# Performance work log

Hardware: AMD Instinct MI355X
Metric: run time of the kernel (lower is better)

The kernel has to match this reference:

```python
import jax, jax.numpy as jnp
import numpy as np

HID = 32

def setup_inputs() -> dict:
    key = jax.random.key(0)
    ks = jax.random.split(key, 20)
    N, F, C, E = 100000, 128, 10, 3200000
    x = jax.random.normal(ks[0], (N, F), dtype=jnp.float32)
    edge_index = jax.random.randint(ks[1], (2, E), 0, N, dtype=jnp.int64)
    edge_weight = jax.random.uniform(ks[2], (E,), dtype=jnp.float32)
    H = jnp.zeros((N, HID), dtype=jnp.float32)
    s = 1.0 / np.sqrt(F)
    t = 1.0 / np.sqrt(2 * HID)
    u = 1.0 / np.sqrt(HID)
    p = {
        'Wz': jax.random.normal(ks[3], (F, HID)) * s,  'bz': jnp.zeros((HID,)),
        'Wr': jax.random.normal(ks[4], (F, HID)) * s,  'br': jnp.zeros((HID,)),
        'Wh': jax.random.normal(ks[5], (F, HID)) * s,  'bh': jnp.zeros((HID,)),
        'Lz_w': jax.random.normal(ks[6], (2 * HID, HID)) * t, 'Lz_b': jnp.zeros((HID,)),
        'Lr_w': jax.random.normal(ks[7], (2 * HID, HID)) * t, 'Lr_b': jnp.zeros((HID,)),
        'Lh_w': jax.random.normal(ks[8], (2 * HID, HID)) * t, 'Lh_b': jnp.zeros((HID,)),
        'lin_w': jax.random.normal(ks[9], (HID, C)) * u,      'lin_b': jnp.zeros((C,)),
    }
    return {'x': x, 'edge_index': edge_index, 'edge_weight': edge_weight, 'H': H, **p}


def reference(x, edge_index, edge_weight, H,
              Wz, bz, Wr, br, Wh, bh,
              Lz_w, Lz_b, Lr_w, Lr_b, Lh_w, Lh_b,
              lin_w, lin_b):
    N = x.shape[0]
    # gcn_norm with self-loops (fill value 1), symmetric normalization
    loop = jnp.arange(N, dtype=edge_index.dtype)
    src = jnp.concatenate([edge_index[0], loop])
    dst = jnp.concatenate([edge_index[1], loop])
    w = jnp.concatenate([edge_weight, jnp.ones((N,), edge_weight.dtype)])
    deg = jax.ops.segment_sum(w, dst, num_segments=N)
    dinv = jnp.where(deg > 0, jax.lax.rsqrt(deg), 0.0)
    norm = dinv[src] * w * dinv[dst]  # [E+N]

    def gcn(W, b):
        xw = x @ W  # [N, HID]
        msg = xw[src] * norm[:, None]  # gather + scale
        return jax.ops.segment_sum(msg, dst, num_segments=N) + b

    Z = jax.nn.sigmoid(jnp.concatenate([gcn(Wz, bz), H], axis=1) @ Lz_w + Lz_b)
    R = jax.nn.sigmoid(jnp.concatenate([gcn(Wr, br), H], axis=1) @ Lr_w + Lr_b)
    H_tilde = jnp.tanh(jnp.concatenate([gcn(Wh, bh), H * R], axis=1) @ Lh_w + Lh_b)
    H_new = Z * H + (1.0 - Z) * H_tilde

    h = jax.nn.relu(H_new)
    logits = h @ lin_w + lin_b
    return (jax.nn.softmax(logits, axis=1), H)
```

## Files before the change

### kernel.cpp

```cpp
#include <hip/hip_runtime.h>
#include <cstdint>
#include <cmath>

#define HID 32
#define GATES 96
#define F 128
#define NB_MAX 512
#define CH 4096
#define STAGE_CAP 9000

typedef float nfloat2 __attribute__((ext_vector_type(2)));

__device__ inline unsigned f2b(float x) {
    unsigned u = __float_as_uint(x);
    return (u + 0x7FFFu + ((u >> 16) & 1u)) >> 16;
}


__global__ __launch_bounds__(256) void k_bcount(const int* __restrict__ ei_dst,
        unsigned* __restrict__ bCnt, int E, int nb) {
    __shared__ unsigned h[NB_MAX];
    for (int i = threadIdx.x; i < NB_MAX; i += 256) h[i] = 0;
    __syncthreads();
    for (int e = blockIdx.x * 256 + threadIdx.x; e < E; e += gridDim.x * 256)
        atomicAdd(&h[((const unsigned*)ei_dst)[e] >> 8], 1u);
    __syncthreads();
    for (int b = threadIdx.x; b < nb; b += 256)
        if (h[b]) atomicAdd(&bCnt[b], h[b]);
}

__global__ __launch_bounds__(512) void k_bscan(const unsigned* __restrict__ bCnt,
        unsigned* __restrict__ bOff, unsigned* __restrict__ bPos, int nb) {
    __shared__ unsigned s[512];
    int t = threadIdx.x;
    unsigned v = (t < nb) ? bCnt[t] : 0u;
    s[t] = v;
    __syncthreads();
    for (int o = 1; o < 512; o <<= 1) {
        unsigned x = s[t];
        if (t >= o) x += s[t - o];
        __syncthreads();
        s[t] = x;
        __syncthreads();
    }
    if (t < nb) { unsigned ex = s[t] - v; bOff[t] = ex; bPos[t] = ex; }
}

__global__ __launch_bounds__(256) void k_bscatter(const int* __restrict__ ei,
        const float* __restrict__ w, unsigned* __restrict__ bPos,
        float2* __restrict__ bsorted, int E) {
    __shared__ unsigned h[NB_MAX], base[NB_MAX];
    int c0 = blockIdx.x * CH;
    int c1 = c0 + CH; if (c1 > E) c1 = E;
    for (int i = threadIdx.x; i < NB_MAX; i += 256) h[i] = 0;
    __syncthreads();
    for (int e = c0 + threadIdx.x; e < c1; e += 256)
        atomicAdd(&h[((const unsigned*)ei)[(size_t)E + e] >> 8], 1u);
    __syncthreads();
    for (int b = threadIdx.x; b < NB_MAX; b += 256) {
        base[b] = h[b] ? atomicAdd(&bPos[b], h[b]) : 0u;
        h[b] = 0;
    }
    __syncthreads();
    for (int e = c0 + threadIdx.x; e < c1; e += 256) {
        unsigned d = ((const unsigned*)ei)[(size_t)E + e];
        unsigned b = d >> 8;
        unsigned r = atomicAdd(&h[b], 1u);
        unsigned pack = (unsigned)ei[e] | ((d & 255u) << 24);
        bsorted[base[b] + r] = make_float2(__int_as_float((int)pack), w[e]);
    }
}

__global__ __launch_bounds__(256) void k_bfine(const float2* __restrict__ bsorted,
        const unsigned* __restrict__ bOff,
        float2* __restrict__ sorted, unsigned* __restrict__ cnt, unsigned* __restrict__ off,
        float* __restrict__ dinv, int N, int E, int nb) {
    __shared__ float2 stage[STAGE_CAP];
    __shared__ unsigned h[256], h2[256], loc[256];
    __shared__ float wsum[256];
    int b = blockIdx.x, t = threadIdx.x;
    unsigned lo = bOff[b];
    unsigned hi = (b + 1 < nb) ? bOff[b + 1] : (unsigned)E;
    unsigned len = hi - lo;
    unsigned stlen = len < STAGE_CAP ? len : STAGE_CAP;
    h[t] = 0; h2[t] = 0; wsum[t] = 0.0f;
    __syncthreads();
    for (unsigned i = t; i < stlen; i += 256) {
        float2 e = bsorted[lo + i];
        stage[i] = e;
        unsigned ld = ((unsigned)__float_as_int(e.x)) >> 24;
        atomicAdd(&h[ld], 1u);
        atomicAdd(&wsum[ld], e.y);
    }
    for (unsigned i = stlen + t; i < len; i += 256) {
        float2 e = bsorted[lo + i];
        unsigned ld = ((unsigned)__float_as_int(e.x)) >> 24;
        atomicAdd(&h[ld], 1u);
        atomicAdd(&wsum[ld], e.y);
    }
    __syncthreads();
    unsigned v = h[t];
    loc[t] = v;
    __syncthreads();
    for (int o = 1; o < 256; o <<= 1) {
        unsigned x = loc[t];
        if (t >= o) x += loc[t - o];
        __syncthreads();
        loc[t] = x;
        __syncthreads();
    }
    unsigned ex = loc[t] - v;
    __syncthreads();
    loc[t] = ex;
    __syncthreads();
    int d = b * 256 + t;
    if (d < N) {
        cnt[d] = v;
        off[d] = lo + ex;
        dinv[d] = rsqrtf(1.0f + wsum[t]);
    }
    for (unsigned i = t; i < stlen; i += 256) {
        float2 e = stage[i];
        unsigned u = (unsigned)__float_as_int(e.x);
        unsigned ld = u >> 24;
        unsigned r = atomicAdd(&h2[ld], 1u);
        sorted[lo + loc[ld] + r] = make_float2(__int_as_float((int)(u & 0xFFFFFFu)), e.y);
    }
    for (unsigned i = stlen + t; i < len; i += 256) {
        float2 e = bsorted[lo + i];
        unsigned u = (unsigned)__float_as_int(e.x);
        unsigned ld = u >> 24;
        unsigned r = atomicAdd(&h2[ld], 1u);
        sorted[lo + loc[ld] + r] = make_float2(__int_as_float((int)(u & 0xFFFFFFu)), e.y);
    }
}

#define GR 16
__global__ __launch_bounds__(256) void k_gemm(const float* __restrict__ x,
        const float* __restrict__ Wz, const float* __restrict__ Wr, const float* __restrict__ Wh,
        const float* __restrict__ dinv, unsigned* __restrict__ xwh, int N) {
    __shared__ float Wl[F * GATES];
    __shared__ float xs[GR][F + 1];
    int tid = threadIdx.x;
    for (int i = tid; i < F * GATES; i += 256) {
        int k = i / GATES, c = i % GATES;
        float v;
        if (c < 32)      v = Wz[k * 32 + c];
        else if (c < 64) v = Wr[k * 32 + (c - 32)];
        else             v = Wh[k * 32 + (c - 64)];
        Wl[i] = v;
    }
    int r_local = tid / 16;
    int cb = tid % 16;
    int ntiles = (N + GR - 1) / GR;
    for (int t = blockIdx.x; t < ntiles; t += gridDim.x) {
        int row0 = t * GR;
        __syncthreads();
        for (int i = tid; i < GR * F; i += 256) {
            int r = i / F, k = i % F;
            int g = row0 + r;
            xs[r][k] = (g < N) ? x[(size_t)g * F + k] : 0.0f;
        }
        __syncthreads();
        int grow = row0 + r_local;
        if (grow < N) {
            float acc[6] = {0, 0, 0, 0, 0, 0};
            for (int k = 0; k < F; ++k) {
                float xv = xs[r_local][k];
                const float* wr = &Wl[k * GATES + cb * 6];
                #pragma unroll
                for (int j = 0; j < 6; ++j) acc[j] += xv * wr[j];
            }
            float dv = dinv[grow];
            unsigned* o = xwh + (size_t)grow * 48 + cb * 3;
            o[0] = f2b(dv * acc[0]) | (f2b(dv * acc[1]) << 16);
            o[1] = f2b(dv * acc[2]) | (f2b(dv * acc[3]) << 16);
            o[2] = f2b(dv * acc[4]) | (f2b(dv * acc[5]) << 16);
        }
    }
}

__global__ __launch_bounds__(256, 8) void k_fused(
        const unsigned* __restrict__ off, const unsigned* __restrict__ cnt,
        const float2* __restrict__ sorted,
        const unsigned* __restrict__ xwh, const float* __restrict__ dinv, const float* __restrict__ Hin,
        const float* __restrict__ bz, const float* __restrict__ br, const float* __restrict__ bh,
        const float* __restrict__ Lzw, const float* __restrict__ Lzb,
        const float* __restrict__ Lrw, const float* __restrict__ Lrb,
        const float* __restrict__ Lhw, const float* __restrict__ Lhb,
        const float* __restrict__ linw, const float* __restrict__ linb,
        float* __restrict__ out_probs, float* __restrict__ out_H, int N) {
    int tid = threadIdx.x;
    int l = tid & 31;
    int half = l >> 4;
    int q = l & 15;
    int n = blockIdx.x * 8 + (tid >> 5);
    if (n >= N) return;

    float di = dinv[n];
    float acc0 = 0, acc1 = 0, acc2 = 0, acc3 = 0, acc4 = 0, acc5 = 0;

    unsigned base = off[n], len = cnt[n];
    const nfloat2* mp = (const nfloat2*)sorted + base;
    unsigned j = half;
    #pragma unroll 2
    for (; j + 2 < len; j += 4) {
        nfloat2 ea = mp[j];
        nfloat2 eb = mp[j + 2];
        int   sa = __float_as_int(ea.x);
        int   sb = __float_as_int(eb.x);
        float ma = ea.y;
        float mb = eb.y;
        const unsigned* pa = xwh + (size_t)sa * 48 + q * 3;
        const unsigned* pb = xwh + (size_t)sb * 48 + q * 3;
        unsigned a0 = pa[0], a1 = pa[1], a2 = pa[2];
        unsigned b0 = pb[0], b1 = pb[1], b2 = pb[2];
        acc0 += ma * __uint_as_float(a0 << 16);
        acc1 += ma * __uint_as_float(a0 & 0xFFFF0000u);
        acc2 += ma * __uint_as_float(a1 << 16);
        acc3 += ma * __uint_as_float(a1 & 0xFFFF0000u);
        acc4 += ma * __uint_as_float(a2 << 16);
        acc5 += ma * __uint_as_float(a2 & 0xFFFF0000u);
        acc0 += mb * __uint_as_float(b0 << 16);
        acc1 += mb * __uint_as_float(b0 & 0xFFFF0000u);
        acc2 += mb * __uint_as_float(b1 << 16);
        acc3 += mb * __uint_as_float(b1 & 0xFFFF0000u);
        acc4 += mb * __uint_as_float(b2 << 16);
        acc5 += mb * __uint_as_float(b2 & 0xFFFF0000u);
    }
    for (; j < len; j += 2) {
        nfloat2 e = mp[j];
        int   s = __float_as_int(e.x);
        float m = e.y;
        const unsigned* p = xwh + (size_t)s * 48 + q * 3;
        unsigned u0 = p[0], u1 = p[1], u2 = p[2];
        acc0 += m * __uint_as_float(u0 << 16);
        acc1 += m * __uint_as_float(u0 & 0xFFFF0000u);
        acc2 += m * __uint_as_float(u1 << 16);
        acc3 += m * __uint_as_float(u1 & 0xFFFF0000u);
        acc4 += m * __uint_as_float(u2 << 16);
        acc5 += m * __uint_as_float(u2 & 0xFFFF0000u);
    }
    acc0 += __shfl_xor(acc0, 16, 32);
    acc1 += __shfl_xor(acc1, 16, 32);
    acc2 += __shfl_xor(acc2, 16, 32);
    acc3 += __shfl_xor(acc3, 16, 32);
    acc4 += __shfl_xor(acc4, 16, 32);
    acc5 += __shfl_xor(acc5, 16, 32);
    float g0, g1, g2, g3, g4, g5;
    {
        const unsigned* p = xwh + (size_t)n * 48 + q * 3;
        unsigned u0 = p[0], u1 = p[1], u2 = p[2];
        #define BIAS(f) ((f) < 32 ? bz[(f)] : ((f) < 64 ? br[(f) - 32] : bh[(f) - 64]))
        int f = q * 6;
        g0 = di * (acc0 + __uint_as_float(u0 << 16))         + BIAS(f);
        g1 = di * (acc1 + __uint_as_float(u0 & 0xFFFF0000u)) + BIAS(f + 1);
        g2 = di * (acc2 + __uint_as_float(u1 << 16))         + BIAS(f + 2);
        g3 = di * (acc3 + __uint_as_float(u1 & 0xFFFF0000u)) + BIAS(f + 3);
        g4 = di * (acc4 + __uint_as_float(u2 << 16))         + BIAS(f + 4);
        g5 = di * (acc5 + __uint_as_float(u2 & 0xFFFF0000u)) + BIAS(f + 5);
        #undef BIAS
    }
    #define GATHERF(out, fexp) { int ff = (fexp); int mm = ff / 6, ii = ff % 6;            \
        float t0 = __shfl(g0, mm, 32), t1 = __shfl(g1, mm, 32), t2 = __shfl(g2, mm, 32),   \
              t3 = __shfl(g3, mm, 32), t4 = __shfl(g4, mm, 32), t5 = __shfl(g5, mm, 32);   \
        out = ii == 0 ? t0 : ii == 1 ? t1 : ii == 2 ? t2 : ii == 3 ? t3 : ii == 4 ? t4 : t5; }
    float gz, gr, gh;
    GATHERF(gz, l);
    GATHERF(gr, 32 + l);
    GATHERF(gh, 64 + l);
    #undef GATHERF

    float Hd = Hin[(size_t)n * HID + l];

    float az = Lzb[l], ar = Lrb[l];
    #pragma unroll 4
    for (int k = 0; k < 32; ++k) {
        float gzk = __shfl(gz, k, 32);
        float grk = __shfl(gr, k, 32);
        float Hk  = __shfl(Hd, k, 32);
        az += gzk * Lzw[k * 32 + l] + Hk * Lzw[(32 + k) * 32 + l];
        ar += grk * Lrw[k * 32 + l] + Hk * Lrw[(32 + k) * 32 + l];
    }
    float Z  = 1.0f / (1.0f + __expf(-az));
    float Rg = 1.0f / (1.0f + __expf(-ar));
    float HR = Hd * Rg;
    float ah = Lhb[l];
    #pragma unroll 4
    for (int k = 0; k < 32; ++k) {
        float ghk = __shfl(gh, k, 32);
        float HRk = __shfl(HR, k, 32);
        ah += ghk * Lhw[k * 32 + l] + HRk * Lhw[(32 + k) * 32 + l];
    }
    float Ht = tanhf(ah);
    float Hn = Z * Hd + (1.0f - Z) * Ht;
    float h = fmaxf(Hn, 0.0f);

    float logit = (l < 10) ? linb[l] : -INFINITY;
    #pragma unroll 4
    for (int k = 0; k < 32; ++k) {
        float hk = __shfl(h, k, 32);
        if (l < 10) logit += hk * linw[k * 10 + l];
    }
    float mx = logit;
    #pragma unroll
    for (int o = 8; o >= 1; o >>= 1) mx = fmaxf(mx, __shfl_xor(mx, o, 16));
    float ex = (l < 10) ? __expf(logit - mx) : 0.0f;
    float sum = ex;
    #pragma unroll
    for (int o = 8; o >= 1; o >>= 1) sum += __shfl_xor(sum, o, 16);
    if (l < 10) out_probs[(size_t)n * 10 + l] = ex / sum;
    out_H[(size_t)n * HID + l] = Hd;
}

extern "C" void kernel_launch(void* const* d_in, const int* in_sizes, int n_in,
                              void* d_out, int out_size, void* d_ws, size_t ws_size,
                              hipStream_t stream) {
    const float* x    = (const float*)d_in[0];
    const int*   ei   = (const int*)d_in[1];
    const float* ew   = (const float*)d_in[2];
    const float* H    = (const float*)d_in[3];
    const float* Wz   = (const float*)d_in[4];
    const float* bz   = (const float*)d_in[5];
    const float* Wr   = (const float*)d_in[6];
    const float* br   = (const float*)d_in[7];
    const float* Wh   = (const float*)d_in[8];
    const float* bh   = (const float*)d_in[9];
    const float* Lzw  = (const float*)d_in[10];
    const float* Lzb  = (const float*)d_in[11];
    const float* Lrw  = (const float*)d_in[12];
    const float* Lrb  = (const float*)d_in[13];
    const float* Lhw  = (const float*)d_in[14];
    const float* Lhb  = (const float*)d_in[15];
    const float* linw = (const float*)d_in[16];
    const float* linb = (const float*)d_in[17];

    int N = in_sizes[0] / F;
    int E = in_sizes[2];
    int nb = (N + 255) / 256;

    float* ws = (float*)d_ws;
    unsigned* xwh     = (unsigned*)ws;
    float2*   sorted  = (float2*)(ws + (size_t)N * 48);
    float2*   bsorted = sorted + (size_t)E;
    float*    dinv    = (float*)(bsorted + (size_t)E);
    unsigned* cnt     = (unsigned*)(dinv + N);
    unsigned* off     = cnt + N;
    unsigned* bCnt    = off + N;
    unsigned* bOff    = bCnt + NB_MAX;
    unsigned* bPos    = bOff + NB_MAX;

    float* out_probs = (float*)d_out;
    float* out_H     = (float*)d_out + (size_t)N * 10;

    hipMemsetAsync(bCnt, 0, NB_MAX * sizeof(unsigned), stream);
    k_bcount<<<512, 256, 0, stream>>>(ei + (size_t)E, bCnt, E, nb);
    k_bscan<<<1, 512, 0, stream>>>(bCnt, bOff, bPos, nb);
    k_bscatter<<<(E + CH - 1) / CH, 256, 0, stream>>>(ei, ew, bPos, bsorted, E);
    k_bfine<<<nb, 256, 0, stream>>>(bsorted, bOff, sorted, cnt, off, dinv, N, E, nb);
    k_gemm<<<2048, 256, 0, stream>>>(x, Wz, Wr, Wh, dinv, xwh, N);
    k_fused<<<(N + 7) / 8, 256, 0, stream>>>(off, cnt, sorted, xwh, dinv, H,
                                             bz, br, bh, Lzw, Lzb, Lrw, Lrb, Lhw, Lhb,
                                             linw, linb, out_probs, out_H, N);
}
```

Before: 410.0 us.

## Fold bucket scan into scatter/fine kernels, cache dst in registers, widen aggregation to 64 lanes

```diff
diff --git a/kernel.cpp b/kernel.cpp
--- a/kernel.cpp
+++ b/kernel.cpp
@@ -7,6 +7,7 @@
 #define F 128
 #define NB_MAX 512
 #define CH 4096
+#define EPT 16
 #define STAGE_CAP 9000
 
 typedef float nfloat2 __attribute__((ext_vector_type(2)));
@@ -15,6 +16,8 @@
     unsigned u = __float_as_uint(x);
     return (u + 0x7FFFu + ((u >> 16) & 1u)) >> 16;
 }
+__device__ inline float blo(unsigned u) { return __uint_as_float(u << 16); }
+__device__ inline float bhi(unsigned u) { return __uint_as_float(u & 0xFFFF0000u); }
 
 
 __global__ __launch_bounds__(256) void k_bcount(const int* __restrict__ ei_dst,
@@ -29,59 +32,76 @@
         if (h[b]) atomicAdd(&bCnt[b], h[b]);
 }
 
-__global__ __launch_bounds__(512) void k_bscan(const unsigned* __restrict__ bCnt,
-        unsigned* __restrict__ bOff, unsigned* __restrict__ bPos, int nb) {
-    __shared__ unsigned s[512];
+__device__ inline void local_bscan(const unsigned* __restrict__ bCnt,
+        unsigned* __restrict__ boff, unsigned* __restrict__ ps) {
     int t = threadIdx.x;
-    unsigned v = (t < nb) ? bCnt[t] : 0u;
-    s[t] = v;
-    __syncthreads();
-    for (int o = 1; o < 512; o <<= 1) {
-        unsigned x = s[t];
-        if (t >= o) x += s[t - o];
-        __syncthreads();
-        s[t] = x;
-        __syncthreads();
-    }
-    if (t < nb) { unsigned ex = s[t] - v; bOff[t] = ex; bPos[t] = ex; }
+    unsigned c0 = bCnt[2 * t], c1 = bCnt[2 * t + 1];
+    unsigned pv = c0 + c1;
+    ps[t] = pv;
+    __syncthreads();
+    for (int o = 1; o < 256; o <<= 1) {
+        unsigned x = ps[t];
+        if (t >= o) x += ps[t - o];
+        __syncthreads();
+        ps[t] = x;
+        __syncthreads();
+    }
+    unsigned pex = ps[t] - pv;
+    boff[2 * t] = pex;
+    boff[2 * t + 1] = pex + c0;
+    __syncthreads();
 }
 
 __global__ __launch_bounds__(256) void k_bscatter(const int* __restrict__ ei,
-        const float* __restrict__ w, unsigned* __restrict__ bPos,
-        float2* __restrict__ bsorted, int E) {
-    __shared__ unsigned h[NB_MAX], base[NB_MAX];
-    int c0 = blockIdx.x * CH;
-    int c1 = c0 + CH; if (c1 > E) c1 = E;
-    for (int i = threadIdx.x; i < NB_MAX; i += 256) h[i] = 0;
-    __syncthreads();
-    for (int e = c0 + threadIdx.x; e < c1; e += 256)
-        atomicAdd(&h[((const unsigned*)ei)[(size_t)E + e] >> 8], 1u);
-    __syncthreads();
-    for (int b = threadIdx.x; b < NB_MAX; b += 256) {
-        base[b] = h[b] ? atomicAdd(&bPos[b], h[b]) : 0u;
+        const float* __restrict__ w, const unsigned* __restrict__ bCnt,
+        unsigned* __restrict__ bPosD, float2* __restrict__ bsorted, int E) {
+    __shared__ unsigned h[NB_MAX], base_[NB_MAX], boff[NB_MAX], ps[256];
+    int t = threadIdx.x;
+    local_bscan(bCnt, boff, ps);
+    for (int i = t; i < NB_MAX; i += 256) h[i] = 0;
+    __syncthreads();
+    int c0e = blockIdx.x * CH;
+    int c1e = c0e + CH; if (c1e > E) c1e = E;
+    unsigned dreg[EPT];
+    #pragma unroll
+    for (int i = 0; i < EPT; ++i) {
+        int e = c0e + i * 256 + t;
+        dreg[i] = 0xFFFFFFFFu;
+        if (e < c1e) {
+            dreg[i] = ((const unsigned*)ei)[(size_t)E + e];
+            atomicAdd(&h[dreg[i] >> 8], 1u);
+        }
+    }
+    __syncthreads();
+    for (int b = t; b < NB_MAX; b += 256) {
+        base_[b] = h[b] ? (boff[b] + atomicAdd(&bPosD[b], h[b])) : 0u;
         h[b] = 0;
     }
     __syncthreads();
-    for (int e = c0 + threadIdx.x; e < c1; e += 256) {
-        unsigned d = ((const unsigned*)ei)[(size_t)E + e];
-        unsigned b = d >> 8;
-        unsigned r = atomicAdd(&h[b], 1u);
-        unsigned pack = (unsigned)ei[e] | ((d & 255u) << 24);
-        bsorted[base[b] + r] = make_float2(__int_as_float((int)pack), w[e]);
+    #pragma unroll
+    for (int i = 0; i < EPT; ++i) {
+        int e = c0e + i * 256 + t;
+        if (e < c1e) {
+            unsigned d = dreg[i];
+            unsigned b = d >> 8;
+            unsigned r = atomicAdd(&h[b], 1u);
+            unsigned pack = (unsigned)ei[e] | ((d & 255u) << 24);
+            bsorted[base_[b] + r] = make_float2(__int_as_float((int)pack), w[e]);
+        }
     }
 }
 
 __global__ __launch_bounds__(256) void k_bfine(const float2* __restrict__ bsorted,
-        const unsigned* __restrict__ bOff,
+        const unsigned* __restrict__ bCnt,
         float2* __restrict__ sorted, unsigned* __restrict__ cnt, unsigned* __restrict__ off,
         float* __restrict__ dinv, int N, int E, int nb) {
     __shared__ float2 stage[STAGE_CAP];
-    __shared__ unsigned h[256], h2[256], loc[256];
+    __shared__ unsigned h[256], h2[256], loc[256], boff[NB_MAX], ps[256];
     __shared__ float wsum[256];
     int b = blockIdx.x, t = threadIdx.x;
-    unsigned lo = bOff[b];
-    unsigned hi = (b + 1 < nb) ? bOff[b + 1] : (unsigned)E;
-    unsigned len = hi - lo;
+    local_bscan(bCnt, boff, ps);
+    unsigned lo = boff[b];
+    unsigned len = bCnt[b];
     unsigned stlen = len < STAGE_CAP ? len : STAGE_CAP;
     h[t] = 0; h2[t] = 0; wsum[t] = 0.0f;
     __syncthreads();
@@ -191,10 +211,10 @@
         const float* __restrict__ linw, const float* __restrict__ linb,
         float* __restrict__ out_probs, float* __restrict__ out_H, int N) {
     int tid = threadIdx.x;
-    int l = tid & 31;
-    int half = l >> 4;
-    int q = l & 15;
-    int n = blockIdx.x * 8 + (tid >> 5);
+    int lane = tid & 63;
+    int sg = lane >> 4;
+    int q = lane & 15;
+    int n = blockIdx.x * 4 + (tid >> 6);
     if (n >= N) return;
 
     float di = dinv[n];
@@ -202,68 +222,44 @@
 
     unsigned base = off[n], len = cnt[n];
     const nfloat2* mp = (const nfloat2*)sorted + base;
-    unsigned j = half;
     #pragma unroll 2
-    for (; j + 2 < len; j += 4) {
-        nfloat2 ea = mp[j];
-        nfloat2 eb = mp[j + 2];
-        int   sa = __float_as_int(ea.x);
-        int   sb = __float_as_int(eb.x);
-        float ma = ea.y;
-        float mb = eb.y;
-        const unsigned* pa = xwh + (size_t)sa * 48 + q * 3;
-        const unsigned* pb = xwh + (size_t)sb * 48 + q * 3;
-        unsigned a0 = pa[0], a1 = pa[1], a2 = pa[2];
-        unsigned b0 = pb[0], b1 = pb[1], b2 = pb[2];
-        acc0 += ma * __uint_as_float(a0 << 16);
-        acc1 += ma * __uint_as_float(a0 & 0xFFFF0000u);
-        acc2 += ma * __uint_as_float(a1 << 16);
-        acc3 += ma * __uint_as_float(a1 & 0xFFFF0000u);
-        acc4 += ma * __uint_as_float(a2 << 16);
-        acc5 += ma * __uint_as_float(a2 & 0xFFFF0000u);
-        acc0 += mb * __uint_as_float(b0 << 16);
-        acc1 += mb * __uint_as_float(b0 & 0xFFFF0000u);
-        acc2 += mb * __uint_as_float(b1 << 16);
-        acc3 += mb * __uint_as_float(b1 & 0xFFFF0000u);
-        acc4 += mb * __uint_as_float(b2 << 16);
-        acc5 += mb * __uint_as_float(b2 & 0xFFFF0000u);
-    }
-    for (; j < len; j += 2) {
+    for (unsigned j = sg; j < len; j += 4) {
         nfloat2 e = mp[j];
         int   s = __float_as_int(e.x);
         float m = e.y;
         const unsigned* p = xwh + (size_t)s * 48 + q * 3;
         unsigned u0 = p[0], u1 = p[1], u2 = p[2];
-        acc0 += m * __uint_as_float(u0 << 16);
-        acc1 += m * __uint_as_float(u0 & 0xFFFF0000u);
-        acc2 += m * __uint_as_float(u1 << 16);
-        acc3 += m * __uint_as_float(u1 & 0xFFFF0000u);
-        acc4 += m * __uint_as_float(u2 << 16);
-        acc5 += m * __uint_as_float(u2 & 0xFFFF0000u);
-    }
-    acc0 += __shfl_xor(acc0, 16, 32);
-    acc1 += __shfl_xor(acc1, 16, 32);
-    acc2 += __shfl_xor(acc2, 16, 32);
-    acc3 += __shfl_xor(acc3, 16, 32);
-    acc4 += __shfl_xor(acc4, 16, 32);
-    acc5 += __shfl_xor(acc5, 16, 32);
+        acc0 += m * blo(u0);
+        acc1 += m * bhi(u0);
+        acc2 += m * blo(u1);
+        acc3 += m * bhi(u1);
+        acc4 += m * blo(u2);
+        acc5 += m * bhi(u2);
+    }
+    acc0 += __shfl_xor(acc0, 16, 64); acc0 += __shfl_xor(acc0, 32, 64);
+    acc1 += __shfl_xor(acc1, 16, 64); acc1 += __shfl_xor(acc1, 32, 64);
+    acc2 += __shfl_xor(acc2, 16, 64); acc2 += __shfl_xor(acc2, 32, 64);
+    acc3 += __shfl_xor(acc3, 16, 64); acc3 += __shfl_xor(acc3, 32, 64);
+    acc4 += __shfl_xor(acc4, 16, 64); acc4 += __shfl_xor(acc4, 32, 64);
+    acc5 += __shfl_xor(acc5, 16, 64); acc5 += __shfl_xor(acc5, 32, 64);
     float g0, g1, g2, g3, g4, g5;
     {
         const unsigned* p = xwh + (size_t)n * 48 + q * 3;
         unsigned u0 = p[0], u1 = p[1], u2 = p[2];
         #define BIAS(f) ((f) < 32 ? bz[(f)] : ((f) < 64 ? br[(f) - 32] : bh[(f) - 64]))
         int f = q * 6;
-        g0 = di * (acc0 + __uint_as_float(u0 << 16))         + BIAS(f);
-        g1 = di * (acc1 + __uint_as_float(u0 & 0xFFFF0000u)) + BIAS(f + 1);
-        g2 = di * (acc2 + __uint_as_float(u1 << 16))         + BIAS(f + 2);
-        g3 = di * (acc3 + __uint_as_float(u1 & 0xFFFF0000u)) + BIAS(f + 3);
-        g4 = di * (acc4 + __uint_as_float(u2 << 16))         + BIAS(f + 4);
-        g5 = di * (acc5 + __uint_as_float(u2 & 0xFFFF0000u)) + BIAS(f + 5);
+        g0 = di * (acc0 + blo(u0)) + BIAS(f);
+        g1 = di * (acc1 + bhi(u0)) + BIAS(f + 1);
+        g2 = di * (acc2 + blo(u1)) + BIAS(f + 2);
+        g3 = di * (acc3 + bhi(u1)) + BIAS(f + 3);
+        g4 = di * (acc4 + blo(u2)) + BIAS(f + 4);
+        g5 = di * (acc5 + bhi(u2)) + BIAS(f + 5);
         #undef BIAS
     }
+    int l = lane & 31;
     #define GATHERF(out, fexp) { int ff = (fexp); int mm = ff / 6, ii = ff % 6;            \
-        float t0 = __shfl(g0, mm, 32), t1 = __shfl(g1, mm, 32), t2 = __shfl(g2, mm, 32),   \
-              t3 = __shfl(g3, mm, 32), t4 = __shfl(g4, mm, 32), t5 = __shfl(g5, mm, 32);   \
+        float t0 = __shfl(g0, mm, 64), t1 = __shfl(g1, mm, 64), t2 = __shfl(g2, mm, 64),   \
+              t3 = __shfl(g3, mm, 64), t4 = __shfl(g4, mm, 64), t5 = __shfl(g5, mm, 64);   \
         out = ii == 0 ? t0 : ii == 1 ? t1 : ii == 2 ? t2 : ii == 3 ? t3 : ii == 4 ? t4 : t5; }
     float gz, gr, gh;
     GATHERF(gz, l);
@@ -309,8 +305,10 @@
     float sum = ex;
     #pragma unroll
     for (int o = 8; o >= 1; o >>= 1) sum += __shfl_xor(sum, o, 16);
-    if (l < 10) out_probs[(size_t)n * 10 + l] = ex / sum;
-    out_H[(size_t)n * HID + l] = Hd;
+    if (lane < 32) {
+        if (l < 10) out_probs[(size_t)n * 10 + l] = ex / sum;
+        out_H[(size_t)n * HID + l] = Hd;
+    }
 }
 
 extern "C" void kernel_launch(void* const* d_in, const int* in_sizes, int n_in,
@@ -347,19 +345,17 @@
     unsigned* cnt     = (unsigned*)(dinv + N);
     unsigned* off     = cnt + N;
     unsigned* bCnt    = off + N;
-    unsigned* bOff    = bCnt + NB_MAX;
-    unsigned* bPos    = bOff + NB_MAX;
+    unsigned* bPosD   = bCnt + NB_MAX;
 
     float* out_probs = (float*)d_out;
     float* out_H     = (float*)d_out + (size_t)N * 10;
 
-    hipMemsetAsync(bCnt, 0, NB_MAX * sizeof(unsigned), stream);
+    hipMemsetAsync(bCnt, 0, 2 * NB_MAX * sizeof(unsigned), stream);
     k_bcount<<<512, 256, 0, stream>>>(ei + (size_t)E, bCnt, E, nb);
-    k_bscan<<<1, 512, 0, stream>>>(bCnt, bOff, bPos, nb);
-    k_bscatter<<<(E + CH - 1) / CH, 256, 0, stream>>>(ei, ew, bPos, bsorted, E);
-    k_bfine<<<nb, 256, 0, stream>>>(bsorted, bOff, sorted, cnt, off, dinv, N, E, nb);
+    k_bscatter<<<(E + CH - 1) / CH, 256, 0, stream>>>(ei, ew, bCnt, bPosD, bsorted, E);
+    k_bfine<<<nb, 256, 0, stream>>>(bsorted, bCnt, sorted, cnt, off, dinv, N, E, nb);
     k_gemm<<<2048, 256, 0, stream>>>(x, Wz, Wr, Wh, dinv, xwh, N);
-    k_fused<<<(N + 7) / 8, 256, 0, stream>>>(off, cnt, sorted, xwh, dinv, H,
+    k_fused<<<(N + 3) / 4, 256, 0, stream>>>(off, cnt, sorted, xwh, dinv, H,
                                              bz, br, bh, Lzw, Lzb, Lrw, Lrb, Lhw, Lhb,
                                              linw, linb, out_probs, out_H, N);
 }
```

After: 528.0 us. 28.8% more time.
